# Performance work log

Measured on AMD Instinct MI355X. Metric: run time of the kernel, lower is better.

Reference implementation:

```python
import jax, jax.numpy as jnp
import numpy as np


def setup_inputs() -> dict:
    key = jax.random.key(0)
    k1, k2, k3 = jax.random.split(key, 3)
    N, E, C, OUT = 100000, 1000000, 64, 64
    x = jax.random.normal(k1, (N, C), dtype=jnp.float32)
    edge_index = jax.random.randint(k2, (2, E), 0, N, dtype=jnp.int32)
    W = jax.random.normal(k3, (2 * C, OUT), dtype=jnp.float32) * (1.0 / np.sqrt(2 * C))
    b = jnp.zeros((OUT,), dtype=jnp.float32)
    return {"x": x, "edge_index": edge_index, "W": W, "b": b}


def reference(x, edge_index, W, b):
    # MRConv: x_j = scatter_max(x[src] - x[dst], dst); out = relu(cat([x, x_j]) @ W + b)
    N = x.shape[0]
    src, dst = edge_index[0], edge_index[1]
    diff = x[src] - x[dst]                                  # [E, C] gather + diff
    x_j = jax.ops.segment_max(diff, dst, num_segments=N)    # [N, C] scatter-max
    # nodes with no incoming edges get -inf from segment_max; tg fills them with 0
    x_j = jnp.where(jnp.isfinite(x_j), x_j, 0.0)
    h = jnp.concatenate([x, x_j], axis=1)                   # [N, 2C]
    return jax.nn.relu(h @ W + b)                           # [N, OUT]
```

## Files before the change

### kernel.cpp

```cpp
#include <hip/hip_runtime.h>
#include <math.h>

#define SENT 0x007FFFFFu
#define NEGINF_BITS 0xFF800000u
#define NA 256
#define SB_SHIFT 5
#define SB_MASK ((1u << SB_SHIFT) - 1u)
#define NB 32
#define PITCH 68
#define MAXSB 4096
#define CG 768
#define PADROW 32u
#define RGRID 2048

typedef __attribute__((ext_vector_type(8))) short bf16x8;
typedef __attribute__((ext_vector_type(4))) float f32x4;

__device__ __forceinline__ unsigned int fmap(float f) {
    unsigned int u = __float_as_uint(f);
    return (u & 0x80000000u) ? ~u : (u | 0x80000000u);
}
__device__ __forceinline__ unsigned int fmap_bits(unsigned int u) {
    return (u & 0x80000000u) ? ~u : (u | 0x80000000u);
}
__device__ __forceinline__ float funmap(unsigned int u) {
    unsigned int bits = (u & 0x80000000u) ? (u ^ 0x80000000u) : ~u;
    return __uint_as_float(bits);
}
__device__ __forceinline__ unsigned short tobf(float f) {
    unsigned int u = __float_as_uint(f);
    u += 0x7FFFu + ((u >> 16) & 1u);
    return (unsigned short)(u >> 16);
}
__device__ __forceinline__ float frombf(unsigned short s) {
    return __uint_as_float((unsigned int)s << 16);
}

__global__ void __launch_bounds__(512) casthist_kernel(const float* __restrict__ x,
                                                       unsigned short* __restrict__ xb,
                                                       long long n,
                                                       const int* __restrict__ ei,
                                                       unsigned* __restrict__ counts2,
                                                       unsigned* __restrict__ ctrl,
                                                       int E, int nsb, int chunk) {
    __shared__ unsigned h[MAXSB];
    if ((int)blockIdx.x < CG) {
        long long i = ((long long)blockIdx.x * 512 + threadIdx.x) * 8;
        long long stride = (long long)CG * 512 * 8;
        for (; i < n; i += stride) {
            float4 a = *(const float4*)(x + i);
            float4 c = *(const float4*)(x + i + 4);
            uint4 o;
            o.x = (unsigned)tobf(a.x) | ((unsigned)tobf(a.y) << 16);
            o.y = (unsigned)tobf(a.z) | ((unsigned)tobf(a.w) << 16);
            o.z = (unsigned)tobf(c.x) | ((unsigned)tobf(c.y) << 16);
            o.w = (unsigned)tobf(c.z) | ((unsigned)tobf(c.w) << 16);
            *(uint4*)(xb + i) = o;
        }
    } else {
        int hb = (int)blockIdx.x - CG;
        if (hb == 0 && threadIdx.x == 0) *ctrl = 0u;
        for (int t = threadIdx.x; t < nsb; t += 512) h[t] = 0u;
        __syncthreads();
        int beg = hb * chunk;
        int end = min(beg + chunk, E);
        for (int i = beg + threadIdx.x; i < end; i += 512)
            atomicAdd(&h[((unsigned)ei[E + i]) >> SB_SHIFT], 1u);
        __syncthreads();
        for (int t = threadIdx.x; t < nsb; t += 512)
            counts2[(size_t)t * NA + hb] = h[t];
    }
}

__global__ void __launch_bounds__(512) histA_kernel(const int* __restrict__ ei,
                                                    unsigned* __restrict__ counts2,
                                                    unsigned* __restrict__ ctrl,
                                                    int E, int nsb, int chunk) {
    __shared__ unsigned h[MAXSB];
    if (blockIdx.x == 0 && threadIdx.x == 0) *ctrl = 0u;
    for (int t = threadIdx.x; t < nsb; t += 512) h[t] = 0u;
    __syncthreads();
    int beg = blockIdx.x * chunk;
    int end = min(beg + chunk, E);
    for (int i = beg + threadIdx.x; i < end; i += 512)
        atomicAdd(&h[((unsigned)ei[E + i]) >> SB_SHIFT], 1u);
    __syncthreads();
    for (int t = threadIdx.x; t < nsb; t += 512)
        counts2[(size_t)t * NA + blockIdx.x] = h[t];
}

__global__ void __launch_bounds__(512) rowscan_kernel(unsigned* __restrict__ counts2,
                                                      unsigned* __restrict__ sbtot,
                                                      unsigned* __restrict__ sbbase,
                                                      unsigned* __restrict__ ctrl, int nsb) {
    __shared__ unsigned wsum[8];
    __shared__ int lastFlag;
    int tid = threadIdx.x;
    int lane = tid & 63;
    int wid = tid >> 6;
    int sb = blockIdx.x * 8 + wid;
    if (sb < nsb) {
        unsigned* row = counts2 + (size_t)sb * NA;
        uint4 v = *(const uint4*)(row + 4 * lane);
        unsigned local = v.x + v.y + v.z + v.w;
        unsigned incl = local;
        #pragma unroll
        for (int d = 1; d < 64; d <<= 1) {
            unsigned t = __shfl_up(incl, d);
            if (lane >= d) incl += t;
        }
        unsigned e0 = incl - local;
        uint4 o;
        o.x = e0;
        o.y = e0 + v.x;
        o.z = o.y + v.y;
        o.w = o.z + v.z;
        *(uint4*)(row + 4 * lane) = o;
        if (lane == 63)
            __hip_atomic_store(&sbtot[sb], incl, __ATOMIC_RELAXED, __HIP_MEMORY_SCOPE_AGENT);
    }
    __syncthreads();
    if (tid == 0) {
        unsigned old = __hip_atomic_fetch_add(ctrl, 1u, __ATOMIC_ACQ_REL, __HIP_MEMORY_SCOPE_AGENT);
        lastFlag = (old == gridDim.x - 1);
    }
    __syncthreads();
    if (!lastFlag) return;

    unsigned excl[8];
    unsigned run = 0;
    #pragma unroll
    for (int i = 0; i < 8; ++i) {
        int idx = tid * 8 + i;
        unsigned c = (idx < nsb)
            ? __hip_atomic_load(&sbtot[idx], __ATOMIC_RELAXED, __HIP_MEMORY_SCOPE_AGENT) : 0u;
        c = (c + 15u) & ~15u;
        excl[i] = run;
        run += c;
    }
    unsigned T = run;
    unsigned incl = T;
    #pragma unroll
    for (int d = 1; d < 64; d <<= 1) {
        unsigned t = __shfl_up(incl, d);
        if (lane >= d) incl += t;
    }
    if (lane == 63) wsum[wid] = incl;
    unsigned texcl = incl - T;
    __syncthreads();
    if (wid == 0) {
        unsigned wv = (lane < 8) ? wsum[lane] : 0u;
        unsigned wincl = wv;
        #pragma unroll
        for (int d = 1; d < 8; d <<= 1) {
            unsigned t = __shfl_up(wincl, d);
            if (lane >= d) wincl += t;
        }
        if (lane < 8) wsum[lane] = wincl - wv;
    }
    __syncthreads();
    unsigned base = wsum[wid] + texcl;
    #pragma unroll
    for (int i = 0; i < 8; ++i) {
        int idx = tid * 8 + i;
        if (idx <= nsb) sbbase[idx] = base + excl[i];
    }
}

__global__ void __launch_bounds__(512) placeB_kernel(const int* __restrict__ ei,
                                                     const unsigned* __restrict__ counts2,
                                                     const unsigned* __restrict__ sbbase,
                                                     const unsigned* __restrict__ sbtot,
                                                     unsigned* __restrict__ ssrc,
                                                     int E, int nsb, int chunk) {
    if ((int)blockIdx.x >= NA) {
        int i = ((int)blockIdx.x - NA) * 512 + threadIdx.x;
        if (i < nsb) {
            unsigned s = sbbase[i] + sbtot[i];
            unsigned e = sbbase[i + 1];
            for (unsigned j = s; j < e; ++j) ssrc[j] = PADROW;
        }
        return;
    }
    __shared__ unsigned fill[MAXSB];
    for (int t = threadIdx.x; t < nsb; t += 512)
        fill[t] = sbbase[t] + counts2[(size_t)t * NA + blockIdx.x];
    __syncthreads();
    int beg = blockIdx.x * chunk;
    int end = min(beg + chunk, E);
    for (int i = beg + threadIdx.x; i < end; i += 512) {
        unsigned src = (unsigned)ei[i];
        unsigned dst = (unsigned)ei[E + i];
        unsigned pos = atomicAdd(&fill[dst >> SB_SHIFT], 1u);
        ssrc[pos] = (src << 6) | (dst & SB_MASK);
    }
}

__global__ void __launch_bounds__(256) reduceBf_kernel(const unsigned short* __restrict__ xb,
                                                       const unsigned* __restrict__ sbbase,
                                                       const unsigned* __restrict__ ssrc,
                                                       unsigned short* __restrict__ xj,
                                                       int N, int nsb) {
    __shared__ unsigned M[(NB + 1) * PITCH];
    int tid = threadIdx.x;
    int lane = tid & 63;
    int wid = tid >> 6;

    for (int sb = blockIdx.x; sb < nsb; sb += gridDim.x) {
        for (int i = tid; i < (NB + 1) * PITCH; i += 256) M[i] = SENT;
        int nodeBase = sb * NB;
        int beg = (int)sbbase[sb];
        int end = (int)sbbase[sb + 1];
        __syncthreads();

        for (int i0 = beg + wid * 16; i0 < end; i0 += 64) {
            int si = __builtin_amdgcn_readfirstlane(i0);
            uint4 q0 = *(const uint4*)(ssrc + si);
            uint4 q1 = *(const uint4*)(ssrc + si + 4);
            uint4 q2 = *(const uint4*)(ssrc + si + 8);
            uint4 q3 = *(const uint4*)(ssrc + si + 12);
            unsigned pp[16] = {q0.x, q0.y, q0.z, q0.w, q1.x, q1.y, q1.z, q1.w,
                               q2.x, q2.y, q2.z, q2.w, q3.x, q3.y, q3.z, q3.w};
            unsigned short vv[16];
            #pragma unroll
            for (int k = 0; k < 16; ++k)
                vv[k] = xb[(pp[k] & 0xFFFFFFC0u) | (unsigned)lane];
            #pragma unroll
            for (int k = 0; k < 16; ++k) {
                unsigned u32 = ((unsigned)vv[k]) << 16;
                atomicMax(&M[(pp[k] & 63u) * PITCH + lane], fmap_bits(u32));
            }
        }
        __syncthreads();

        for (int row = wid; row < NB; row += 4) {
            int n = nodeBase + row;
            if (n < N) {
                unsigned um = M[row * PITCH + lane];
                unsigned short o = 0;
                if (um != SENT) {
                    float mx = funmap(um);
                    float xv = frombf(xb[(size_t)n * 64 + lane]);
                    o = tobf(mx - xv);
                }
                xj[(size_t)n * 64 + lane] = o;
            }
        }
        __syncthreads();
    }
}

__global__ void __launch_bounds__(256) mlpBf_kernel(const unsigned short* __restrict__ xb,
                                                    const unsigned short* __restrict__ xj,
                                                    const float* __restrict__ W,
                                                    const float* __restrict__ b,
                                                    float* __restrict__ out, int N) {
    int lane = threadIdx.x & 63;
    int wid  = threadIdx.x >> 6;
    int r = lane & 15;
    int g = lane >> 4;

    bf16x8 Bf[4][4];
    #pragma unroll
    for (int nt = 0; nt < 4; ++nt)
        #pragma unroll
        for (int kt = 0; kt < 4; ++kt) {
            const float* wp = W + (size_t)(kt * 32 + g * 8) * 64 + nt * 16 + r;
            bf16x8 f;
            #pragma unroll
            for (int j = 0; j < 8; ++j) f[j] = (short)tobf(wp[(size_t)j * 64]);
            Bf[nt][kt] = f;
        }
    float bias[4];
    #pragma unroll
    for (int nt = 0; nt < 4; ++nt) bias[nt] = b[nt * 16 + r];

    int nTiles = (N + 15) >> 4;
    int totalWaves = gridDim.x * 4;
    for (int tile = blockIdx.x * 4 + wid; tile < nTiles; tile += totalWaves) {
        int nodeBase = tile << 4;
        int rowIdx = min(nodeBase + r, N - 1);
        const unsigned short* xp = xb + (size_t)rowIdx * 64;
        const unsigned short* jp = xj + (size_t)rowIdx * 64;

        bf16x8 Af[4];
        #pragma unroll
        for (int kt = 0; kt < 2; ++kt) {
            Af[kt]     = *(const bf16x8*)(xp + kt * 32 + g * 8);
            Af[2 + kt] = *(const bf16x8*)(jp + kt * 32 + g * 8);
        }

        f32x4 acc[4];
        #pragma unroll
        for (int nt = 0; nt < 4; ++nt) {
            f32x4 a = {bias[nt], bias[nt], bias[nt], bias[nt]};
            acc[nt] = a;
        }
        #pragma unroll
        for (int nt = 0; nt < 4; ++nt)
            #pragma unroll
            for (int kt = 0; kt < 4; ++kt)
                acc[nt] = __builtin_amdgcn_mfma_f32_16x16x32_bf16(Af[kt], Bf[nt][kt], acc[nt], 0, 0, 0);

        #pragma unroll
        for (int nt = 0; nt < 4; ++nt)
            #pragma unroll
            for (int reg = 0; reg < 4; ++reg) {
                int nrow = nodeBase + g * 4 + reg;
                if (nrow < N)
                    out[(size_t)nrow * 64 + nt * 16 + r] = fmaxf(acc[nt][reg], 0.0f);
            }
    }
}


__global__ void __launch_bounds__(256) reduceB_kernel(const float* __restrict__ x,
                                                      const unsigned* __restrict__ sbbase,
                                                      const unsigned* __restrict__ ssrc,
                                                      float* __restrict__ xj, int N) {
    __shared__ unsigned M[(NB + 1) * PITCH];
    int tid = threadIdx.x;
    int lane = tid & 63;
    int wid = tid >> 6;

    for (int i = tid; i < (NB + 1) * PITCH; i += 256) M[i] = SENT;

    int nodeBase = blockIdx.x * NB;
    int beg = (int)sbbase[blockIdx.x];
    int end = (int)sbbase[blockIdx.x + 1];
    __syncthreads();

    for (int i0 = beg + wid * 16; i0 < end; i0 += 64) {
        int si = __builtin_amdgcn_readfirstlane(i0);
        uint4 q0 = *(const uint4*)(ssrc + si);
        uint4 q1 = *(const uint4*)(ssrc + si + 4);
        uint4 q2 = *(const uint4*)(ssrc + si + 8);
        uint4 q3 = *(const uint4*)(ssrc + si + 12);
        unsigned pp[16] = {q0.x, q0.y, q0.z, q0.w, q1.x, q1.y, q1.z, q1.w,
                           q2.x, q2.y, q2.z, q2.w, q3.x, q3.y, q3.z, q3.w};
        float vv[16];
        #pragma unroll
        for (int k = 0; k < 16; ++k)
            vv[k] = x[(pp[k] & 0xFFFFFFC0u) | (unsigned)lane];
        #pragma unroll
        for (int k = 0; k < 16; ++k)
            atomicMax(&M[(pp[k] & 63u) * PITCH + lane], fmap(vv[k]));
    }
    __syncthreads();

    for (int row = wid; row < NB; row += 4) {
        int n = nodeBase + row;
        if (n < N) xj[(size_t)n * 64 + lane] = funmap(M[row * PITCH + lane]);
    }
}

template <bool MAPPED>
__global__ void __launch_bounds__(256) mlp_kernel(const float* __restrict__ x,
                                                  const unsigned int* xj,
                                                  const float* __restrict__ W,
                                                  const float* __restrict__ b,
                                                  float* out, int N) {
    int lane = threadIdx.x & 63;
    int wid  = threadIdx.x >> 6;
    int r = lane & 15;
    int g = lane >> 4;

    bf16x8 Bf[4][4];
    #pragma unroll
    for (int nt = 0; nt < 4; ++nt)
        #pragma unroll
        for (int kt = 0; kt < 4; ++kt) {
            const float* wp = W + (size_t)(kt * 32 + g * 8) * 64 + nt * 16 + r;
            bf16x8 f;
            #pragma unroll
            for (int j = 0; j < 8; ++j) f[j] = (short)tobf(wp[(size_t)j * 64]);
            Bf[nt][kt] = f;
        }
    float bias[4];
    #pragma unroll
    for (int nt = 0; nt < 4; ++nt) bias[nt] = b[nt * 16 + r];

    int nTiles = (N + 15) >> 4;
    int totalWaves = gridDim.x * 4;
    for (int tile = blockIdx.x * 4 + wid; tile < nTiles; tile += totalWaves) {
        int nodeBase = tile << 4;
        int rowIdx = min(nodeBase + r, N - 1);
        const float* xp = x + (size_t)rowIdx * 64;
        const unsigned int* jp = xj + (size_t)rowIdx * 64;

        bf16x8 Af[4];
        float xs[2][8];
        #pragma unroll
        for (int kt = 0; kt < 2; ++kt) {
            float4 flo = *(const float4*)(xp + kt * 32 + g * 8);
            float4 fhi = *(const float4*)(xp + kt * 32 + g * 8 + 4);
            xs[kt][0] = flo.x; xs[kt][1] = flo.y; xs[kt][2] = flo.z; xs[kt][3] = flo.w;
            xs[kt][4] = fhi.x; xs[kt][5] = fhi.y; xs[kt][6] = fhi.z; xs[kt][7] = fhi.w;
            bf16x8 f;
            #pragma unroll
            for (int j = 0; j < 8; ++j) f[j] = (short)tobf(xs[kt][j]);
            Af[kt] = f;
        }
        #pragma unroll
        for (int kt = 0; kt < 2; ++kt) {
            uint4 ulo = *(const uint4*)(jp + kt * 32 + g * 8);
            uint4 uhi = *(const uint4*)(jp + kt * 32 + g * 8 + 4);
            unsigned int uu[8] = {ulo.x, ulo.y, ulo.z, ulo.w, uhi.x, uhi.y, uhi.z, uhi.w};
            bf16x8 f;
            #pragma unroll
            for (int j = 0; j < 8; ++j) {
                bool empty;
                float v;
                if (MAPPED) { empty = (uu[j] == SENT); v = funmap(uu[j]); }
                else        { empty = (uu[j] == NEGINF_BITS); v = __uint_as_float(uu[j]); }
                f[j] = (short)tobf(empty ? 0.0f : (v - xs[kt][j]));
            }
            Af[2 + kt] = f;
        }

        f32x4 acc[4];
        #pragma unroll
        for (int nt = 0; nt < 4; ++nt) {
            f32x4 a = {bias[nt], bias[nt], bias[nt], bias[nt]};
            acc[nt] = a;
        }
        #pragma unroll
        for (int nt = 0; nt < 4; ++nt)
            #pragma unroll
            for (int kt = 0; kt < 4; ++kt)
                acc[nt] = __builtin_amdgcn_mfma_f32_16x16x32_bf16(Af[kt], Bf[nt][kt], acc[nt], 0, 0, 0);

        #pragma unroll
        for (int nt = 0; nt < 4; ++nt)
            #pragma unroll
            for (int reg = 0; reg < 4; ++reg) {
                int nrow = nodeBase + g * 4 + reg;
                if (nrow < N)
                    out[(size_t)nrow * 64 + nt * 16 + r] = fmaxf(acc[nt][reg], 0.0f);
            }
    }
}


__global__ void init_kernel(uint4* __restrict__ ws, int n4) {
    int i = blockIdx.x * blockDim.x + threadIdx.x;
    int stride = gridDim.x * blockDim.x;
    uint4 v = make_uint4(SENT, SENT, SENT, SENT);
    for (; i < n4; i += stride) ws[i] = v;
}

__global__ void scatter_kernel(const float* __restrict__ x,
                               const int* __restrict__ ei,
                               unsigned int* __restrict__ ws, int E) {
    long long gid = (long long)blockIdx.x * blockDim.x + threadIdx.x;
    int e = (int)(gid >> 6);
    int lane = (int)(gid & 63);
    if (e >= E) return;
    int src = ei[e];
    int dst = ei[E + e];
    unsigned int m = fmap(x[(size_t)src * 64 + lane]);
    unsigned int* p = ws + (size_t)dst * 64 + lane;
    if (m > *p) atomicMax(p, m);
}

extern "C" void kernel_launch(void* const* d_in, const int* in_sizes, int n_in,
                              void* d_out, int out_size, void* d_ws, size_t ws_size,
                              hipStream_t stream) {
    const float* x  = (const float*)d_in[0];
    const int*   ei = (const int*)d_in[1];
    const float* W  = (const float*)d_in[2];
    const float* b  = (const float*)d_in[3];
    float* out = (float*)d_out;

    int N = in_sizes[0] / 64;
    int E = in_sizes[1] / 2;

    int nsb = (N + NB - 1) >> SB_SHIFT;
    int chunk = (E + NA - 1) / NA;
    int padB = (nsb + 511) / 512;

    size_t counts2_b = (size_t)nsb * NA * 4;
    size_t sbtot_b   = (size_t)((nsb + 63) & ~63) * 4;
    size_t sbbase_b  = (size_t)(nsb + 1 + 63) / 64 * 64 * 4;
    size_t ctrl_b    = 64;
    size_t ssrc_b    = ((size_t)E + 16u * (size_t)nsb) * 4;
    size_t xb_b      = (size_t)N * 64 * 2;
    size_t xjb_b     = (size_t)N * 64 * 2;
    size_t xj32_b    = (size_t)N * 64 * 4;
    size_t needB     = counts2_b + sbtot_b + sbbase_b + ctrl_b + ssrc_b;
    size_t needA     = needB + xb_b + xjb_b;

    int mgrid = (((N + 15) >> 4) + 3) / 4;
    int rsgrid = (nsb + 7) / 8;

    if (ws_size >= needA && nsb <= MAXSB) {
        char* p = (char*)d_ws;
        unsigned* counts2 = (unsigned*)p; p += counts2_b;
        unsigned* sbtot   = (unsigned*)p; p += sbtot_b;
        unsigned* sbbase  = (unsigned*)p; p += sbbase_b;
        unsigned* ctrl    = (unsigned*)p; p += ctrl_b;
        unsigned* ssrc    = (unsigned*)p; p += ssrc_b;
        unsigned short* xb  = (unsigned short*)p; p += xb_b;
        unsigned short* xjb = (unsigned short*)p;

        long long n = (long long)N * 64;
        casthist_kernel<<<CG + NA, 512, 0, stream>>>(x, xb, n, ei, counts2, ctrl, E, nsb, chunk);
        rowscan_kernel<<<rsgrid, 512, 0, stream>>>(counts2, sbtot, sbbase, ctrl, nsb);
        placeB_kernel<<<NA + padB, 512, 0, stream>>>(ei, counts2, sbbase, sbtot, ssrc, E, nsb, chunk);
        int rgrid = (nsb < RGRID) ? nsb : RGRID;
        reduceBf_kernel<<<rgrid, 256, 0, stream>>>(xb, sbbase, ssrc, xjb, N, nsb);
        mlpBf_kernel<<<mgrid, 256, 0, stream>>>(xb, xjb, W, b, out, N);
    } else if (ws_size >= needB && nsb <= MAXSB) {
        char* p = (char*)d_ws;
        unsigned* counts2 = (unsigned*)p; p += counts2_b;
        unsigned* sbtot   = (unsigned*)p; p += sbtot_b;
        unsigned* sbbase  = (unsigned*)p; p += sbbase_b;
        unsigned* ctrl    = (unsigned*)p; p += ctrl_b;
        unsigned* ssrc    = (unsigned*)p; p += ssrc_b;
        float* xjp = (ws_size >= needB + xj32_b) ? (float*)p : (float*)d_out;

        histA_kernel<<<NA, 512, 0, stream>>>(ei, counts2, ctrl, E, nsb, chunk);
        rowscan_kernel<<<rsgrid, 512, 0, stream>>>(counts2, sbtot, sbbase, ctrl, nsb);
        placeB_kernel<<<NA + padB, 512, 0, stream>>>(ei, counts2, sbbase, sbtot, ssrc, E, nsb, chunk);
        reduceB_kernel<<<nsb, 256, 0, stream>>>(x, sbbase, ssrc, xjp, N);
        mlp_kernel<false><<<mgrid, 256, 0, stream>>>(x, (const unsigned*)xjp, W, b, out, N);
    } else {
        size_t need2 = (size_t)N * 64 * 4;
        unsigned int* scratch = (ws_size >= need2) ? (unsigned int*)d_ws : (unsigned int*)d_out;
        init_kernel<<<2048, 256, 0, stream>>>((uint4*)scratch, N * 16);
        long long sthreads = (long long)E * 64;
        int sblocks = (int)((sthreads + 255) / 256);
        scatter_kernel<<<sblocks, 256, 0, stream>>>(x, ei, scratch, E);
        mlp_kernel<true><<<mgrid, 256, 0, stream>>>(x, scratch, W, b, out, N);
    }
}
```

Measured before the change: 94.67 us.

## Fuse scatter-max reduction with bf16 MFMA linear layer in one kernel

The separate reduce and MLP kernels are merged. Each block builds x_j for its 32 nodes in shared memory, then two waves run the 16x16x32 bf16 MFMAs straight from that shared tile, with the bf16 weights staged once per block in LDS. This drops the bf16 x_j round trip through global memory and one kernel launch. In exchange only two of four waves do the matmul phase, and the block pays extra LDS and per-block weight conversion.

```diff
diff --git a/kernel.cpp b/kernel.cpp
--- a/kernel.cpp
+++ b/kernel.cpp
@@ -196,15 +196,34 @@
     }
 }
 
-__global__ void __launch_bounds__(256) reduceBf_kernel(const unsigned short* __restrict__ xb,
-                                                       const unsigned* __restrict__ sbbase,
-                                                       const unsigned* __restrict__ ssrc,
-                                                       unsigned short* __restrict__ xj,
-                                                       int N, int nsb) {
+__global__ void __launch_bounds__(256) fusedRM_kernel(const unsigned short* __restrict__ xb,
+                                                      const unsigned* __restrict__ sbbase,
+                                                      const unsigned* __restrict__ ssrc,
+                                                      const float* __restrict__ W,
+                                                      const float* __restrict__ b,
+                                                      float* __restrict__ out,
+                                                      int N, int nsb) {
     __shared__ unsigned M[(NB + 1) * PITCH];
+    __shared__ unsigned short Wf[4][4][64][8];
     int tid = threadIdx.x;
     int lane = tid & 63;
     int wid = tid >> 6;
+    int r = lane & 15;
+    int g = lane >> 4;
+
+    for (int idx = tid; idx < 1024; idx += 256) {
+        int kt = idx >> 8;
+        int nt = (idx >> 6) & 3;
+        int l  = idx & 63;
+        int k0 = kt * 32 + ((l >> 4) << 3);
+        int nn = nt * 16 + (l & 15);
+        unsigned short* dst = &Wf[kt][nt][l][0];
+        #pragma unroll
+        for (int j = 0; j < 8; ++j) dst[j] = tobf(W[(size_t)(k0 + j) * 64 + nn]);
+    }
+    float bias[4];
+    #pragma unroll
+    for (int nt = 0; nt < 4; ++nt) bias[nt] = b[nt * 16 + r];
 
     for (int sb = blockIdx.x; sb < nsb; sb += gridDim.x) {
         for (int i = tid; i < (NB + 1) * PITCH; i += 256) M[i] = SENT;
@@ -233,83 +252,56 @@
         }
         __syncthreads();
 
-        for (int row = wid; row < NB; row += 4) {
-            int n = nodeBase + row;
-            if (n < N) {
-                unsigned um = M[row * PITCH + lane];
-                unsigned short o = 0;
-                if (um != SENT) {
-                    float mx = funmap(um);
-                    float xv = frombf(xb[(size_t)n * 64 + lane]);
-                    o = tobf(mx - xv);
+        if (wid < 2) {
+            int tb = nodeBase + wid * 16;
+            int rowIdx = min(tb + r, N - 1);
+            const unsigned short* xp = xb + (size_t)rowIdx * 64;
+            int lrow = wid * 16 + r;
+
+            bf16x8 Af[4];
+            #pragma unroll
+            for (int kt = 0; kt < 2; ++kt)
+                Af[kt] = *(const bf16x8*)(xp + kt * 32 + g * 8);
+            #pragma unroll
+            for (int kt = 0; kt < 2; ++kt) {
+                int ch0 = kt * 32 + g * 8;
+                uint4 ulo = *(const uint4*)&M[lrow * PITCH + ch0];
+                uint4 uhi = *(const uint4*)&M[lrow * PITCH + ch0 + 4];
+                unsigned uu[8] = {ulo.x, ulo.y, ulo.z, ulo.w, uhi.x, uhi.y, uhi.z, uhi.w};
+                bf16x8 f;
+                #pragma unroll
+                for (int j = 0; j < 8; ++j) {
+                    bool empty = (uu[j] == SENT);
+                    float xv = frombf((unsigned short)Af[kt][j]);
+                    f[j] = (short)tobf(empty ? 0.0f : (funmap(uu[j]) - xv));
                 }
-                xj[(size_t)n * 64 + lane] = o;
+                Af[2 + kt] = f;
             }
+
+            f32x4 acc[4];
+            #pragma unroll
+            for (int nt = 0; nt < 4; ++nt) {
+                f32x4 a = {bias[nt], bias[nt], bias[nt], bias[nt]};
+                acc[nt] = a;
+            }
+            #pragma unroll
+            for (int nt = 0; nt < 4; ++nt)
+                #pragma unroll
+                for (int kt = 0; kt < 4; ++kt) {
+                    bf16x8 bf = *(const bf16x8*)&Wf[kt][nt][lane][0];
+                    acc[nt] = __builtin_amdgcn_mfma_f32_16x16x32_bf16(Af[kt], bf, acc[nt], 0, 0, 0);
+                }
+
+            #pragma unroll
+            for (int nt = 0; nt < 4; ++nt)
+                #pragma unroll
+                for (int reg = 0; reg < 4; ++reg) {
+                    int nrow = tb + g * 4 + reg;
+                    if (nrow < N)
+                        out[(size_t)nrow * 64 + nt * 16 + r] = fmaxf(acc[nt][reg], 0.0f);
+                }
         }
         __syncthreads();
-    }
-}
-
-__global__ void __launch_bounds__(256) mlpBf_kernel(const unsigned short* __restrict__ xb,
-                                                    const unsigned short* __restrict__ xj,
-                                                    const float* __restrict__ W,
-                                                    const float* __restrict__ b,
-                                                    float* __restrict__ out, int N) {
-    int lane = threadIdx.x & 63;
-    int wid  = threadIdx.x >> 6;
-    int r = lane & 15;
-    int g = lane >> 4;
-
-    bf16x8 Bf[4][4];
-    #pragma unroll
-    for (int nt = 0; nt < 4; ++nt)
-        #pragma unroll
-        for (int kt = 0; kt < 4; ++kt) {
-            const float* wp = W + (size_t)(kt * 32 + g * 8) * 64 + nt * 16 + r;
-            bf16x8 f;
-            #pragma unroll
-            for (int j = 0; j < 8; ++j) f[j] = (short)tobf(wp[(size_t)j * 64]);
-            Bf[nt][kt] = f;
-        }
-    float bias[4];
-    #pragma unroll
-    for (int nt = 0; nt < 4; ++nt) bias[nt] = b[nt * 16 + r];
-
-    int nTiles = (N + 15) >> 4;
-    int totalWaves = gridDim.x * 4;
-    for (int tile = blockIdx.x * 4 + wid; tile < nTiles; tile += totalWaves) {
-        int nodeBase = tile << 4;
-        int rowIdx = min(nodeBase + r, N - 1);
-        const unsigned short* xp = xb + (size_t)rowIdx * 64;
-        const unsigned short* jp = xj + (size_t)rowIdx * 64;
-
-        bf16x8 Af[4];
-        #pragma unroll
-        for (int kt = 0; kt < 2; ++kt) {
-            Af[kt]     = *(const bf16x8*)(xp + kt * 32 + g * 8);
-            Af[2 + kt] = *(const bf16x8*)(jp + kt * 32 + g * 8);
-        }
-
-        f32x4 acc[4];
-        #pragma unroll
-        for (int nt = 0; nt < 4; ++nt) {
-            f32x4 a = {bias[nt], bias[nt], bias[nt], bias[nt]};
-            acc[nt] = a;
-        }
-        #pragma unroll
-        for (int nt = 0; nt < 4; ++nt)
-            #pragma unroll
-            for (int kt = 0; kt < 4; ++kt)
-                acc[nt] = __builtin_amdgcn_mfma_f32_16x16x32_bf16(Af[kt], Bf[nt][kt], acc[nt], 0, 0, 0);
-
-        #pragma unroll
-        for (int nt = 0; nt < 4; ++nt)
-            #pragma unroll
-            for (int reg = 0; reg < 4; ++reg) {
-                int nrow = nodeBase + g * 4 + reg;
-                if (nrow < N)
-                    out[(size_t)nrow * 64 + nt * 16 + r] = fmaxf(acc[nt][reg], 0.0f);
-            }
     }
 }
 
@@ -485,10 +477,9 @@
     size_t ctrl_b    = 64;
     size_t ssrc_b    = ((size_t)E + 16u * (size_t)nsb) * 4;
     size_t xb_b      = (size_t)N * 64 * 2;
-    size_t xjb_b     = (size_t)N * 64 * 2;
     size_t xj32_b    = (size_t)N * 64 * 4;
     size_t needB     = counts2_b + sbtot_b + sbbase_b + ctrl_b + ssrc_b;
-    size_t needA     = needB + xb_b + xjb_b;
+    size_t needA     = needB + xb_b;
 
     int mgrid = (((N + 15) >> 4) + 3) / 4;
     int rsgrid = (nsb + 7) / 8;
@@ -500,16 +491,14 @@
         unsigned* sbbase  = (unsigned*)p; p += sbbase_b;
         unsigned* ctrl    = (unsigned*)p; p += ctrl_b;
         unsigned* ssrc    = (unsigned*)p; p += ssrc_b;
-        unsigned short* xb  = (unsigned short*)p; p += xb_b;
-        unsigned short* xjb = (unsigned short*)p;
+        unsigned short* xb = (unsigned short*)p;
 
         long long n = (long long)N * 64;
         casthist_kernel<<<CG + NA, 512, 0, stream>>>(x, xb, n, ei, counts2, ctrl, E, nsb, chunk);
         rowscan_kernel<<<rsgrid, 512, 0, stream>>>(counts2, sbtot, sbbase, ctrl, nsb);
         placeB_kernel<<<NA + padB, 512, 0, stream>>>(ei, counts2, sbbase, sbtot, ssrc, E, nsb, chunk);
         int rgrid = (nsb < RGRID) ? nsb : RGRID;
-        reduceBf_kernel<<<rgrid, 256, 0, stream>>>(xb, sbbase, ssrc, xjb, N, nsb);
-        mlpBf_kernel<<<mgrid, 256, 0, stream>>>(xb, xjb, W, b, out, N);
+        fusedRM_kernel<<<rgrid, 256, 0, stream>>>(xb, sbbase, ssrc, W, b, out, N, nsb);
     } else if (ws_size >= needB && nsb <= MAXSB) {
         char* p = (char*)d_ws;
         unsigned* counts2 = (unsigned*)p; p += counts2_b;
```

Measured after the change: 87.22 us, median of 2. 7.9% less time.
